# Optimization experiments

Measured on AMD Instinct MI355X. Metric: run time of the kernel, lower is better.

Reference implementation:

```python
import jax, jax.numpy as jnp
import numpy as np

N_NODES = 20000
N_EDGES = 320000
NODE_DIM = 512
HIDDEN = 512
N_GRAPHS = 64


def setup_inputs() -> dict:
    key = jax.random.key(0)
    ks = jax.random.split(key, 12)
    s = 0.02
    return {
        "joint_x": jax.random.normal(ks[0], (N_NODES, NODE_DIM), jnp.float32),
        "joint_edge_index": jax.random.randint(ks[1], (2, N_EDGES), 0, N_NODES, dtype=jnp.int32),
        "joint_batch": jnp.sort(jax.random.randint(ks[2], (N_NODES,), 0, N_GRAPHS, dtype=jnp.int32)),
        "W_g1": jax.random.normal(ks[3], (NODE_DIM, HIDDEN), jnp.float32) * s,
        "b_g1": jnp.zeros((HIDDEN,), jnp.float32),
        "W_g2": jax.random.normal(ks[4], (HIDDEN, HIDDEN), jnp.float32) * s,
        "b_g2": jnp.zeros((HIDDEN,), jnp.float32),
        "W_c1": jax.random.normal(ks[5], (HIDDEN, HIDDEN // 2), jnp.float32) * s,
        "b_c1": jnp.zeros((HIDDEN // 2,), jnp.float32),
        "W_c2": jax.random.normal(ks[6], (HIDDEN // 2, 1), jnp.float32) * s,
        "b_c2": jnp.zeros((1,), jnp.float32),
    }


def _gin_layer(h, src, dst, W, b):
    # GINConv(nn=Linear, eps=0): nn((1+eps)*x_i + sum_{j->i} x_j)
    agg = jax.ops.segment_sum(h[src], dst, num_segments=N_NODES)  # [N, D]
    return (h + agg) @ W + b


def reference(joint_x, joint_edge_index, joint_batch, W_g1, b_g1, W_g2, b_g2, W_c1, b_c1, W_c2, b_c2):
    src, dst = joint_edge_index[0], joint_edge_index[1]
    h = _gin_layer(joint_x, src, dst, W_g1, b_g1)  # [N, HIDDEN]
    h = _gin_layer(h, src, dst, W_g2, b_g2)        # [N, HIDDEN]
    pooled = jax.ops.segment_sum(h, joint_batch, num_segments=N_GRAPHS)  # [G, HIDDEN]
    z = jax.nn.relu(pooled @ W_c1 + b_c1)
    score = z @ W_c2 + b_c2                        # [G, 1]
    return jax.nn.sigmoid(score).squeeze(-1)       # [G]
```

## Files before the change

kernel.cpp:

```cpp
#include <hip/hip_runtime.h>
#include <math.h>

constexpr int N_NODES = 20000;
constexpr int DIM = 512;
constexpr int NG = 64;
constexpr int CAP = 64;
constexpr int KCH = 128;
constexpr int NCHUNK = (N_NODES + KCH - 1) / KCH;
constexpr int RSPLIT = 4;
constexpr int CPS = (NCHUNK + RSPLIT - 1) / RSPLIT;
constexpr int CGS = 32;
constexpr int CSTR = 16;
constexpr int NODE_BLOCKS = (N_NODES + 3) / 4;
constexpr int GEMM_TILES = 17 * 4;
constexpr int EPT = 4;
constexpr int EDGE_BLOCKS = (320000 + 256 * EPT - 1) / (256 * EPT);

__device__ __forceinline__ int lower_bound_i(const int* __restrict__ a, int n, int v) {
  int lo = 0, hi = n;
  while (lo < hi) {
    int mid = (lo + hi) >> 1;
    if (a[mid] < v) lo = mid + 1; else hi = mid;
  }
  return lo;
}

__global__ __launch_bounds__(256) void node_init(const int* __restrict__ batch,
                                                 float* __restrict__ wT,
                                                 int* __restrict__ cursor,
                                                 float* __restrict__ ng,
                                                 float* __restrict__ cgpad, int n_nodes) {
  int node = blockIdx.x * 4 + (threadIdx.x >> 6);
  int g = threadIdx.x & 63;
  if (node < n_nodes) {
    int b = batch[node];
    wT[(size_t)node * 64 + g] = (g == b) ? 1.f : 0.f;
    if (g == 0) cursor[(size_t)node * CSTR] = 0;
  }
  if (blockIdx.x == 0 && threadIdx.x < 64) {
    int gg = threadIdx.x;
    int s0 = lower_bound_i(batch, n_nodes, gg);
    int e0 = lower_bound_i(batch, n_nodes, gg + 1);
    ng[gg] = (float)(e0 - s0);
    cgpad[gg * CGS] = 0.f;
  }
}

__device__ void gemm_stack_tile(const float* __restrict__ A0, const float* __restrict__ extra,
                                const float* __restrict__ B, float* __restrict__ C,
                                int M, int N, int K, int R0, int tile,
                                float* As, float* Bs, int tid) {
  int bm = (tile >> 2) * 32;
  int bn = (tile & 3) * 64;
  int tx = tid & 15;
  int ty = tid >> 4;
  int ar = tid >> 3;
  int ac = (tid & 7) * 2;
  int br = tid >> 4;
  int bc = (tid & 15) * 4;
  float acc[2][4] = {};
  for (int k0 = 0; k0 < K; k0 += 16) {
    int row = bm + ar;
    float2 av = make_float2(0.f, 0.f);
    if (row < R0)       av = *(const float2*)(A0 + (size_t)row * K + k0 + ac);
    else if (row == R0) av = *(const float2*)(extra + k0 + ac);
    As[(ac + 0) * 34 + ar] = av.x;
    As[(ac + 1) * 34 + ar] = av.y;
    *(float4*)&Bs[br * 68 + bc] = *(const float4*)(B + (size_t)(k0 + br) * N + bn + bc);
    __syncthreads();
#pragma unroll
    for (int kk = 0; kk < 16; ++kk) {
      float2 a01 = *(const float2*)&As[kk * 34 + ty * 2];
      float4 bv  = *(const float4*)&Bs[kk * 68 + tx * 4];
      acc[0][0] = fmaf(a01.x, bv.x, acc[0][0]); acc[0][1] = fmaf(a01.x, bv.y, acc[0][1]);
      acc[0][2] = fmaf(a01.x, bv.z, acc[0][2]); acc[0][3] = fmaf(a01.x, bv.w, acc[0][3]);
      acc[1][0] = fmaf(a01.y, bv.x, acc[1][0]); acc[1][1] = fmaf(a01.y, bv.y, acc[1][1]);
      acc[1][2] = fmaf(a01.y, bv.z, acc[1][2]); acc[1][3] = fmaf(a01.y, bv.w, acc[1][3]);
    }
    __syncthreads();
  }
#pragma unroll
  for (int i = 0; i < 2; ++i) {
    int m = bm + ty * 2 + i;
    if (m >= M) continue;
    *(float4*)&C[(size_t)m * N + bn + tx * 4] =
        make_float4(acc[i][0], acc[i][1], acc[i][2], acc[i][3]);
  }
}

__global__ __launch_bounds__(256) void fill_and_Q(const int* __restrict__ srcI,
                                                  const int* __restrict__ dstI,
                                                  const int* __restrict__ batch,
                                                  int* __restrict__ cursor,
                                                  int* __restrict__ edst,
                                                  float* __restrict__ wT,
                                                  float* __restrict__ cgpad,
                                                  const float* __restrict__ Wg2,
                                                  const float* __restrict__ bg2,
                                                  const float* __restrict__ Wc1,
                                                  float* __restrict__ Q, int n_edges) {
  __shared__ float As[16 * 34];
  __shared__ float Bs[16 * 68];
  __shared__ int hist[64];
  int b = blockIdx.x;
  int t = threadIdx.x;
  if (b < EDGE_BLOCKS) {
    if (t < 64) hist[t] = 0;
    __syncthreads();
    int base = b * (256 * EPT) + t;
    int s[EPT], d[EPT], c[EPT], bb[EPT];
    bool v[EPT];
#pragma unroll
    for (int u = 0; u < EPT; ++u) {
      int i = base + u * 256;
      v[u] = i < n_edges;
      s[u] = v[u] ? srcI[i] : 0;
    }
#pragma unroll
    for (int u = 0; u < EPT; ++u) {
      int i = base + u * 256;
      d[u] = v[u] ? dstI[i] : 0;
    }
#pragma unroll
    for (int u = 0; u < EPT; ++u)
      if (v[u]) c[u] = atomicAdd(&cursor[(size_t)s[u] * CSTR], 1);
#pragma unroll
    for (int u = 0; u < EPT; ++u) bb[u] = v[u] ? batch[d[u]] : 0;
#pragma unroll
    for (int u = 0; u < EPT; ++u)
      if (v[u]) edst[(size_t)s[u] * CAP + c[u]] = d[u];
#pragma unroll
    for (int u = 0; u < EPT; ++u)
      if (v[u]) {
        atomicAdd(&wT[(size_t)s[u] * 64 + bb[u]], 1.f);
        atomicAdd(&hist[bb[u]], 1);
      }
    __syncthreads();
    if (t < 64 && hist[t] != 0) atomicAdd(&cgpad[t * CGS], (float)hist[t]);
  } else {
    gemm_stack_tile(Wg2, bg2, Wc1, Q, 513, 256, 512, 512, b - EDGE_BLOCKS, As, Bs, t);
  }
}

__global__ __launch_bounds__(256) void cT_and_P(const float* __restrict__ wT,
                                                const int* __restrict__ deg,
                                                const int* __restrict__ edst,
                                                float* __restrict__ cT,
                                                const float* __restrict__ Wg1,
                                                const float* __restrict__ bg1,
                                                const float* __restrict__ Q,
                                                float* __restrict__ P, int n_nodes) {
  __shared__ float As[16 * 34];
  __shared__ float Bs[16 * 68];
  int b = blockIdx.x;
  int t = threadIdx.x;
  if (b < NODE_BLOCKS) {
    int node = b * 4 + (t >> 6);
    int g = t & 63;
    if (node >= n_nodes) return;
    float acc = wT[(size_t)node * 64 + g];
    int end = deg[(size_t)node * CSTR];
    const int* nb = edst + (size_t)node * CAP;
    int i = 0;
    for (; i + 7 < end; i += 8) {
      int d0 = nb[i], d1 = nb[i + 1], d2 = nb[i + 2], d3 = nb[i + 3];
      int d4 = nb[i + 4], d5 = nb[i + 5], d6 = nb[i + 6], d7 = nb[i + 7];
      float v0 = wT[(size_t)d0 * 64 + g], v1 = wT[(size_t)d1 * 64 + g];
      float v2 = wT[(size_t)d2 * 64 + g], v3 = wT[(size_t)d3 * 64 + g];
      float v4 = wT[(size_t)d4 * 64 + g], v5 = wT[(size_t)d5 * 64 + g];
      float v6 = wT[(size_t)d6 * 64 + g], v7 = wT[(size_t)d7 * 64 + g];
      acc += ((v0 + v1) + (v2 + v3)) + ((v4 + v5) + (v6 + v7));
    }
    for (; i + 3 < end; i += 4) {
      int d0 = nb[i], d1 = nb[i + 1], d2 = nb[i + 2], d3 = nb[i + 3];
      acc += wT[(size_t)d0 * 64 + g] + wT[(size_t)d1 * 64 + g] +
             wT[(size_t)d2 * 64 + g] + wT[(size_t)d3 * 64 + g];
    }
    for (; i < end; ++i) acc += wT[(size_t)nb[i] * 64 + g];
    cT[(size_t)node * 64 + g] = acc;
  } else {
    gemm_stack_tile(Wg1, bg1, Q, P, 513, 256, 512, 512, b - NODE_BLOCKS, As, Bs, t);
  }
}

__global__ __launch_bounds__(256) void ugemm(const float* __restrict__ x,
                                             const float* __restrict__ cT,
                                             float* __restrict__ Upart) {
  __shared__ float sc[KCH][64];
  int t = threadIdx.x;
  int k0 = blockIdx.y * KCH;
  int kmax = (N_NODES - k0) < KCH ? (N_NODES - k0) : KCH;
  {
    const float4* src = (const float4*)(cT + (size_t)k0 * 64);
    float4* dst = (float4*)(&sc[0][0]);
    int limit4 = kmax * 16;
    for (int i = t; i < limit4; i += 256) dst[i] = src[i];
  }
  __syncthreads();
  int lane = t & 63;
  int slice = t >> 6;
  int n2 = blockIdx.x * 64 + lane;
  const float2* x2 = (const float2*)x;
  float2 acc[16];
#pragma unroll
  for (int j = 0; j < 16; ++j) acc[j] = make_float2(0.f, 0.f);
  for (int kk = 0; kk < kmax; kk += 4) {
    float2 xv[4];
#pragma unroll
    for (int u = 0; u < 4; ++u)
      xv[u] = x2[(size_t)(k0 + kk + u) * 256 + n2];
#pragma unroll
    for (int u = 0; u < 4; ++u) {
      const float4* cp = (const float4*)&sc[kk + u][slice * 16];
      float4 c0 = cp[0], c1 = cp[1], c2 = cp[2], c3 = cp[3];
      float2 xu = xv[u];
      acc[0].x  = fmaf(c0.x, xu.x, acc[0].x);  acc[0].y  = fmaf(c0.x, xu.y, acc[0].y);
      acc[1].x  = fmaf(c0.y, xu.x, acc[1].x);  acc[1].y  = fmaf(c0.y, xu.y, acc[1].y);
      acc[2].x  = fmaf(c0.z, xu.x, acc[2].x);  acc[2].y  = fmaf(c0.z, xu.y, acc[2].y);
      acc[3].x  = fmaf(c0.w, xu.x, acc[3].x);  acc[3].y  = fmaf(c0.w, xu.y, acc[3].y);
      acc[4].x  = fmaf(c1.x, xu.x, acc[4].x);  acc[4].y  = fmaf(c1.x, xu.y, acc[4].y);
      acc[5].x  = fmaf(c1.y, xu.x, acc[5].x);  acc[5].y  = fmaf(c1.y, xu.y, acc[5].y);
      acc[6].x  = fmaf(c1.z, xu.x, acc[6].x);  acc[6].y  = fmaf(c1.z, xu.y, acc[6].y);
      acc[7].x  = fmaf(c1.w, xu.x, acc[7].x);  acc[7].y  = fmaf(c1.w, xu.y, acc[7].y);
      acc[8].x  = fmaf(c2.x, xu.x, acc[8].x);  acc[8].y  = fmaf(c2.x, xu.y, acc[8].y);
      acc[9].x  = fmaf(c2.y, xu.x, acc[9].x);  acc[9].y  = fmaf(c2.y, xu.y, acc[9].y);
      acc[10].x = fmaf(c2.z, xu.x, acc[10].x); acc[10].y = fmaf(c2.z, xu.y, acc[10].y);
      acc[11].x = fmaf(c2.w, xu.x, acc[11].x); acc[11].y = fmaf(c2.w, xu.y, acc[11].y);
      acc[12].x = fmaf(c3.x, xu.x, acc[12].x); acc[12].y = fmaf(c3.x, xu.y, acc[12].y);
      acc[13].x = fmaf(c3.y, xu.x, acc[13].x); acc[13].y = fmaf(c3.y, xu.y, acc[13].y);
      acc[14].x = fmaf(c3.z, xu.x, acc[14].x); acc[14].y = fmaf(c3.z, xu.y, acc[14].y);
      acc[15].x = fmaf(c3.w, xu.x, acc[15].x); acc[15].y = fmaf(c3.w, xu.y, acc[15].y);
    }
  }
  float2* up = (float2*)Upart;
#pragma unroll
  for (int j = 0; j < 16; ++j) {
    int g = slice * 16 + j;
    up[((size_t)blockIdx.y * 64 + g) * 256 + n2] = acc[j];
  }
}

__global__ __launch_bounds__(128) void reduce_U(const float* __restrict__ Upart,
                                                float* __restrict__ Ured) {
  int g = blockIdx.x;
  int s = blockIdx.y;
  int t = threadIdx.x;
  int c0 = s * CPS;
  int c1 = (c0 + CPS < NCHUNK) ? c0 + CPS : NCHUNK;
  const float4* up = (const float4*)Upart;
  float4 acc = make_float4(0.f, 0.f, 0.f, 0.f);
  for (int c = c0; c < c1; ++c) {
    float4 v = up[((size_t)c * 64 + g) * 128 + t];
    acc.x += v.x; acc.y += v.y; acc.z += v.z; acc.w += v.w;
  }
  ((float4*)Ured)[((size_t)s * 64 + g) * 128 + t] = acc;
}

__global__ __launch_bounds__(256) void head(const float* __restrict__ Ured,
                                            const float* __restrict__ P,
                                            const float* __restrict__ Q,
                                            const float* __restrict__ ng,
                                            const float* __restrict__ cgpad,
                                            const float* __restrict__ bc1,
                                            const float* __restrict__ Wc2,
                                            const float* __restrict__ bc2,
                                            float* __restrict__ out) {
  int g = blockIdx.x;
  int j = threadIdx.x;
  const float* Wc = P;
  const float* v1 = P + (size_t)512 * 256;
  const float* v2 = Q + (size_t)512 * 256;
  __shared__ float p[512];
  float s0 = 0.f, s1 = 0.f;
#pragma unroll
  for (int s = 0; s < RSPLIT; ++s) {
    s0 += Ured[((size_t)s * 64 + g) * DIM + j];
    s1 += Ured[((size_t)s * 64 + g) * DIM + 256 + j];
  }
  p[j] = s0;
  p[j + 256] = s1;
  __syncthreads();
  float cg = ng[g] + cgpad[g * CGS];
  float acc = bc1[j] + cg * v1[j] + ng[g] * v2[j];
  for (int k = 0; k < 512; ++k) acc = fmaf(p[k], Wc[k * 256 + j], acc);
  float z = fmaxf(acc, 0.f);
  float part = z * Wc2[j];
  for (int off = 32; off > 0; off >>= 1) part += __shfl_down(part, off, 64);
  __shared__ float red[4];
  if ((j & 63) == 0) red[j >> 6] = part;
  __syncthreads();
  if (j == 0) {
    float tot = red[0] + red[1] + red[2] + red[3] + bc2[0];
    out[g] = 1.f / (1.f + expf(-tot));
  }
}

extern "C" void kernel_launch(void* const* d_in, const int* in_sizes, int n_in,
                              void* d_out, int out_size, void* d_ws, size_t ws_size,
                              hipStream_t stream) {
  const float* x    = (const float*)d_in[0];
  const int*   ei   = (const int*)d_in[1];
  const int*   batch= (const int*)d_in[2];
  const float* Wg1  = (const float*)d_in[3];
  const float* bg1  = (const float*)d_in[4];
  const float* Wg2  = (const float*)d_in[5];
  const float* bg2  = (const float*)d_in[6];
  const float* Wc1  = (const float*)d_in[7];
  const float* bc1  = (const float*)d_in[8];
  const float* Wc2  = (const float*)d_in[9];
  const float* bc2  = (const float*)d_in[10];
  float* out = (float*)d_out;

  int n_edges = in_sizes[1] / 2;
  int n_nodes = in_sizes[2];
  const int* srcI = ei;
  const int* dstI = ei + n_edges;

  char* ws = (char*)d_ws;
  size_t off = 0;
  auto alloc = [&](size_t bytes) { char* p = ws + off; off += (bytes + 255) & ~(size_t)255; return p; };
  float* wT    = (float*)alloc((size_t)N_NODES * 64 * sizeof(float));
  float* cT    = (float*)alloc((size_t)N_NODES * 64 * sizeof(float));
  float* Upart = (float*)alloc((size_t)NCHUNK * 64 * DIM * sizeof(float));
  float* Ured  = (float*)alloc((size_t)RSPLIT * 64 * DIM * sizeof(float));
  float* Q     = (float*)alloc((size_t)513 * 256 * sizeof(float));
  float* P     = (float*)alloc((size_t)513 * 256 * sizeof(float));
  float* ng    = (float*)alloc(NG * sizeof(float));
  float* cgpad = (float*)alloc(NG * CGS * sizeof(float));
  int* cursor  = (int*)alloc((size_t)N_NODES * CSTR * sizeof(int));
  int* edst    = (int*)alloc((size_t)N_NODES * CAP * sizeof(int));

  node_init<<<NODE_BLOCKS, 256, 0, stream>>>(batch, wT, cursor, ng, cgpad, n_nodes);
  fill_and_Q<<<EDGE_BLOCKS + GEMM_TILES, 256, 0, stream>>>(srcI, dstI, batch, cursor, edst,
                                                           wT, cgpad, Wg2, bg2, Wc1, Q, n_edges);
  cT_and_P<<<NODE_BLOCKS + GEMM_TILES, 256, 0, stream>>>(wT, cursor, edst, cT,
                                                         Wg1, bg1, Q, P, n_nodes);
  ugemm<<<dim3(4, NCHUNK), 256, 0, stream>>>(x, cT, Upart);
  reduce_U<<<dim3(64, RSPLIT), 128, 0, stream>>>(Upart, Ured);
  head<<<NG, 256, 0, stream>>>(Ured, P, Q, ng, cgpad, bc1, Wc2, bc2, out);
}
```

Measured before the change: 233.9 us.

## Build per-node graph-count matrix from adjacency lists instead of scattered float atomics

Stops the edge-fill kernel from zero-initialising wT and doing a global float atomicAdd per edge into it. A new build_wT kernel computes each node's 64-wide graph-count row by walking the node's adjacency list and comparing neighbour batch IDs, writing each entry once. The edge kernel also processes 2 edges per thread instead of 4. This removes contended global atomics and a full init pass, at the cost of an extra kernel launch and repeated reads of edst and batch by all 64 lanes per node.

```diff
diff --git a/kernel.cpp b/kernel.cpp
--- a/kernel.cpp
+++ b/kernel.cpp
@@ -12,8 +12,9 @@
 constexpr int CGS = 32;
 constexpr int CSTR = 16;
 constexpr int NODE_BLOCKS = (N_NODES + 3) / 4;
+constexpr int INIT_BLOCKS = (N_NODES + 255) / 256;
 constexpr int GEMM_TILES = 17 * 4;
-constexpr int EPT = 4;
+constexpr int EPT = 2;
 constexpr int EDGE_BLOCKS = (320000 + 256 * EPT - 1) / (256 * EPT);
 
 __device__ __forceinline__ int lower_bound_i(const int* __restrict__ a, int n, int v) {
@@ -26,17 +27,11 @@
 }
 
 __global__ __launch_bounds__(256) void node_init(const int* __restrict__ batch,
-                                                 float* __restrict__ wT,
                                                  int* __restrict__ cursor,
                                                  float* __restrict__ ng,
                                                  float* __restrict__ cgpad, int n_nodes) {
-  int node = blockIdx.x * 4 + (threadIdx.x >> 6);
-  int g = threadIdx.x & 63;
-  if (node < n_nodes) {
-    int b = batch[node];
-    wT[(size_t)node * 64 + g] = (g == b) ? 1.f : 0.f;
-    if (g == 0) cursor[(size_t)node * CSTR] = 0;
-  }
+  int node = blockIdx.x * 256 + threadIdx.x;
+  if (node < n_nodes) cursor[(size_t)node * CSTR] = 0;
   if (blockIdx.x == 0 && threadIdx.x < 64) {
     int gg = threadIdx.x;
     int s0 = lower_bound_i(batch, n_nodes, gg);
@@ -93,7 +88,6 @@
                                                   const int* __restrict__ batch,
                                                   int* __restrict__ cursor,
                                                   int* __restrict__ edst,
-                                                  float* __restrict__ wT,
                                                   float* __restrict__ cgpad,
                                                   const float* __restrict__ Wg2,
                                                   const float* __restrict__ bg2,
@@ -108,7 +102,7 @@
     if (t < 64) hist[t] = 0;
     __syncthreads();
     int base = b * (256 * EPT) + t;
-    int s[EPT], d[EPT], c[EPT], bb[EPT];
+    int s[EPT], d[EPT], c[EPT];
     bool v[EPT];
 #pragma unroll
     for (int u = 0; u < EPT; ++u) {
@@ -125,21 +119,39 @@
     for (int u = 0; u < EPT; ++u)
       if (v[u]) c[u] = atomicAdd(&cursor[(size_t)s[u] * CSTR], 1);
 #pragma unroll
-    for (int u = 0; u < EPT; ++u) bb[u] = v[u] ? batch[d[u]] : 0;
-#pragma unroll
     for (int u = 0; u < EPT; ++u)
       if (v[u]) edst[(size_t)s[u] * CAP + c[u]] = d[u];
 #pragma unroll
     for (int u = 0; u < EPT; ++u)
-      if (v[u]) {
-        atomicAdd(&wT[(size_t)s[u] * 64 + bb[u]], 1.f);
-        atomicAdd(&hist[bb[u]], 1);
-      }
+      if (v[u]) atomicAdd(&hist[batch[d[u]]], 1);
     __syncthreads();
     if (t < 64 && hist[t] != 0) atomicAdd(&cgpad[t * CGS], (float)hist[t]);
   } else {
     gemm_stack_tile(Wg2, bg2, Wc1, Q, 513, 256, 512, 512, b - EDGE_BLOCKS, As, Bs, t);
   }
+}
+
+__global__ __launch_bounds__(256) void build_wT(const int* __restrict__ batch,
+                                                const int* __restrict__ deg,
+                                                const int* __restrict__ edst,
+                                                float* __restrict__ wT, int n_nodes) {
+  int node = blockIdx.x * 4 + (threadIdx.x >> 6);
+  int g = threadIdx.x & 63;
+  if (node >= n_nodes) return;
+  int end = deg[(size_t)node * CSTR];
+  const int* nb = edst + (size_t)node * CAP;
+  float acc = (batch[node] == g) ? 1.f : 0.f;
+  int i = 0;
+  for (; i + 7 < end; i += 8) {
+    int d0 = nb[i], d1 = nb[i + 1], d2 = nb[i + 2], d3 = nb[i + 3];
+    int d4 = nb[i + 4], d5 = nb[i + 5], d6 = nb[i + 6], d7 = nb[i + 7];
+    int b0 = batch[d0], b1 = batch[d1], b2 = batch[d2], b3 = batch[d3];
+    int b4 = batch[d4], b5 = batch[d5], b6 = batch[d6], b7 = batch[d7];
+    acc += ((float)(b0 == g) + (float)(b1 == g)) + ((float)(b2 == g) + (float)(b3 == g)) +
+           ((float)(b4 == g) + (float)(b5 == g)) + ((float)(b6 == g) + (float)(b7 == g));
+  }
+  for (; i < end; ++i) acc += (float)(batch[nb[i]] == g);
+  wT[(size_t)node * 64 + g] = acc;
 }
 
 __global__ __launch_bounds__(256) void cT_and_P(const float* __restrict__ wT,
@@ -330,9 +342,10 @@
   int* cursor  = (int*)alloc((size_t)N_NODES * CSTR * sizeof(int));
   int* edst    = (int*)alloc((size_t)N_NODES * CAP * sizeof(int));
 
-  node_init<<<NODE_BLOCKS, 256, 0, stream>>>(batch, wT, cursor, ng, cgpad, n_nodes);
+  node_init<<<INIT_BLOCKS, 256, 0, stream>>>(batch, cursor, ng, cgpad, n_nodes);
   fill_and_Q<<<EDGE_BLOCKS + GEMM_TILES, 256, 0, stream>>>(srcI, dstI, batch, cursor, edst,
-                                                           wT, cgpad, Wg2, bg2, Wc1, Q, n_edges);
+                                                           cgpad, Wg2, bg2, Wc1, Q, n_edges);
+  build_wT<<<NODE_BLOCKS, 256, 0, stream>>>(batch, cursor, edst, wT, n_nodes);
   cT_and_P<<<NODE_BLOCKS + GEMM_TILES, 256, 0, stream>>>(wT, cursor, edst, cT,
                                                          Wg1, bg1, Q, P, n_nodes);
   ugemm<<<dim3(4, NCHUNK), 256, 0, stream>>>(x, cT, Upart);
```

Result: slower. 244.5 us (+4.5%).
